# Kernel tuning notes

Hardware: AMD Instinct MI355X
Metric: run time of the kernel (lower is better)

Reference implementation:

```python
import jax, jax.numpy as jnp
import numpy as np

# ---- static config (mirrors init_kwargs) ----
B, N, C_IN, C_OUT = 4, 8192, 128, 256
RATIO = 0.25
M = int(N * RATIO)          # sampled centers per cloud (fps ratio)
RADIUS = 0.1
MAX_NN = 64                 # max_num_neighbors
K = 16                      # num kernel points
D_MID = C_IN // 2           # pre_mlp: in_features -> in_features // 2
KP_EXTENT = RADIUS          # kernel-point influence extent (linear influence)


def setup_inputs() -> dict:
    key = jax.random.key(0)
    ks = jax.random.split(key, 10)
    x = jax.random.normal(ks[0], (B, N, C_IN), jnp.float32)
    pos = jax.random.uniform(ks[1], (B, N, 3), jnp.float32)  # unit cube
    W_pre = jax.random.normal(ks[2], (C_IN, D_MID), jnp.float32) / np.sqrt(C_IN).astype(np.float32)
    b_pre = jnp.zeros((D_MID,), jnp.float32)
    kp_pos = jax.random.normal(ks[3], (K, 3), jnp.float32) * (0.3 * RADIUS)
    kp_W = jax.random.normal(ks[4], (K, D_MID, D_MID), jnp.float32) / np.sqrt(D_MID * K).astype(np.float32)
    W_post = jax.random.normal(ks[5], (D_MID, C_OUT), jnp.float32) / np.sqrt(D_MID).astype(np.float32)
    b_post = jnp.zeros((C_OUT,), jnp.float32)
    W_sc = jax.random.normal(ks[6], (C_IN, C_OUT), jnp.float32) / np.sqrt(C_IN).astype(np.float32)
    b_sc = jnp.zeros((C_OUT,), jnp.float32)
    return dict(x=x, pos=pos, W_pre=W_pre, b_pre=b_pre, kp_pos=kp_pos, kp_W=kp_W,
                W_post=W_post, b_post=b_post, W_sc=W_sc, b_sc=b_sc)


def _fps(p):
    """Farthest point sampling on one cloud p:[N,3] -> idx:[M] (start at point 0)."""
    mind = jnp.sum((p - p[0]) ** 2, axis=-1)  # [N]
    def step(mind, _):
        i = jnp.argmax(mind).astype(jnp.int32)
        mind = jnp.minimum(mind, jnp.sum((p - p[i]) ** 2, axis=-1))
        return mind, i
    _, rest = jax.lax.scan(step, mind, None, length=M - 1)
    return jnp.concatenate([jnp.zeros((1,), jnp.int32), rest])


def reference(x, pos, W_pre, b_pre, kp_pos, kp_W, W_post, b_post, W_sc, b_sc):
    def _cloud(xb, pb):
        # xb:[N,C_IN], pb:[N,3]
        idx = _fps(pb)                                   # [M]
        centers = pb[idx]                                # [M,3]
        # radius neighbor search: nearest MAX_NN, mask to ball of RADIUS
        d2 = jnp.sum((centers[:, None, :] - pb[None, :, :]) ** 2, axis=-1)   # [M,N]
        neg_d2, nn_idx = jax.lax.top_k(-d2, MAX_NN)      # [M,MAX_NN]
        valid = (-neg_d2) <= RADIUS ** 2                 # [M,MAX_NN]
        # pre mlp then gather neighbor features (x_j)
        x_pre = xb @ W_pre + b_pre                       # [N,D_MID]
        x_j = x_pre[nn_idx]                              # [M,MAX_NN,D_MID]
        # kernel-point conv: linear influence of each kernel point
        rel = pb[nn_idx] - centers[:, None, :]           # [M,MAX_NN,3]
        dist = jnp.sqrt(jnp.sum((rel[:, :, None, :] - kp_pos[None, None, :, :]) ** 2, axis=-1) + 1e-12)  # [M,MAX_NN,K]
        infl = jnp.maximum(1.0 - dist / KP_EXTENT, 0.0) * valid[:, :, None]
        # aggregate (sum over neighbors) per kernel point, then contract with kernel weights
        s = jnp.einsum('mek,med->mkd', infl, x_j)        # [M,K,D_MID]
        feat = jnp.einsum('mkd,kdo->mo', s, kp_W)        # [M,D_MID]
        feat = feat @ W_post + b_post                    # [M,C_OUT]
        short = xb[idx] @ W_sc + b_sc                    # residual shortcut on sampled points
        return feat + short, centers

    out_feat, out_pos = jax.vmap(_cloud)(x, pos)         # [B,M,C_OUT], [B,M,3]
    return out_feat, out_pos
```

## Files before the change

### kernel.cpp

```cpp
#include <hip/hip_runtime.h>

#define B_    4
#define N_    8192
#define CIN   128
#define COUT  256
#define M_    2048
#define K_    16
#define DM    64
#define MAXNN 64
#define CAP   128
#define R2    0.01f
#define EXT   0.1f

#define NPRE  1024
#define CONV0 (4 + NPRE)
#define PUB   32

typedef float v2f __attribute__((ext_vector_type(2)));
typedef unsigned long long ull;

__device__ __forceinline__ float d2_exact(float ax, float ay, float az,
                                          float bx, float by, float bz) {
    float dx = ax - bx, dy = ay - by, dz = az - bz;
    return __fadd_rn(__fadd_rn(__fmul_rn(dx, dx), __fmul_rn(dy, dy)), __fmul_rn(dz, dz));
}

#define DPP_STEP2(CTRL)                                                                   \
    {                                                                                     \
        unsigned tlo = (unsigned)__builtin_amdgcn_update_dpp(0, (int)klo, CTRL, 0xF, 0xF, true); \
        unsigned thi = (unsigned)__builtin_amdgcn_update_dpp(0, (int)khi, CTRL, 0xF, 0xF, true); \
        unsigned long long tk = ((unsigned long long)thi << 32) | tlo;                    \
        unsigned long long ck = ((unsigned long long)khi << 32) | klo;                    \
        if (tk > ck) { klo = tlo; khi = thi; }                                            \
    }

__global__ void init_kernel(int* __restrict__ flags) {
    if (threadIdx.x < 8) flags[threadIdx.x] = 0;
}

__global__ __launch_bounds__(512, 2) void mega_kernel(const float* __restrict__ pos,
                                                      int* __restrict__ idx_out,
                                                      float* __restrict__ out_pos,
                                                      const float* __restrict__ x,
                                                      const float* __restrict__ Wp,
                                                      const float* __restrict__ bvec,
                                                      float* __restrict__ xpre,
                                                      const float* __restrict__ kp_pos,
                                                      const float* __restrict__ kp_W,
                                                      const float* __restrict__ W_post,
                                                      const float* __restrict__ b_post,
                                                      const float* __restrict__ W_sc,
                                                      const float* __restrict__ b_sc,
                                                      float* __restrict__ out_feat,
                                                      int* __restrict__ flags) {
    __shared__ union {
        struct { float sx[N_]; float sy[N_]; float sz[N_]; ull slots[2][8]; } f;
        struct { float Ws[CIN * DM]; float xs[32][CIN]; } p;
        struct { int nIdx[CAP]; float nD2[CAP]; int cntS;
                 float infl[MAXNN][K_]; float xj[MAXNN][DM];
                 float sS[K_ * DM]; float featP[4][DM]; float xg[CIN]; } c;
    } sh;

    const int t = threadIdx.x;
    const int blk = blockIdx.x;

    if (blk >= CONV0) {
        const int cid = blk - CONV0;
        const int cb = cid & 3;
        const int cm = cid >> 2;

        if (t == 0) {
            while (__hip_atomic_load(&flags[cb], __ATOMIC_RELAXED, __HIP_MEMORY_SCOPE_AGENT) <= cm ||
                   __hip_atomic_load(&flags[4], __ATOMIC_RELAXED, __HIP_MEMORY_SCOPE_AGENT) < NPRE) {
                __builtin_amdgcn_s_sleep(64);
            }
            __threadfence();
            sh.c.cntS = 0;
        }
        __syncthreads();

        const float* pb = pos + (size_t)cb * N_ * 3;
        const int ctr = idx_out[cb * M_ + cm];
        const float ccx = pb[ctr * 3 + 0], ccy = pb[ctr * 3 + 1], ccz = pb[ctr * 3 + 2];

        for (int j = 0; j < N_ / 512; j++) {
            int n = j * 512 + t;
            float x0 = pb[n * 3 + 0], y0 = pb[n * 3 + 1], z0 = pb[n * 3 + 2];
            float d = d2_exact(x0, y0, z0, ccx, ccy, ccz);
            if (d <= R2) {
                int pp = atomicAdd(&sh.c.cntS, 1);
                if (pp < CAP) { sh.c.nIdx[pp] = n; sh.c.nD2[pp] = d; }
            }
        }
        __syncthreads();
        int cnt = sh.c.cntS; if (cnt > CAP) cnt = CAP;
        if (cnt > MAXNN) {
            if (t == 0) {
                for (int s = 0; s < MAXNN; s++) {
                    int best = s;
                    for (int q = s + 1; q < cnt; q++) {
                        if (sh.c.nD2[q] < sh.c.nD2[best] ||
                            (sh.c.nD2[q] == sh.c.nD2[best] && sh.c.nIdx[q] < sh.c.nIdx[best])) best = q;
                    }
                    float td = sh.c.nD2[best]; sh.c.nD2[best] = sh.c.nD2[s]; sh.c.nD2[s] = td;
                    int ti = sh.c.nIdx[best]; sh.c.nIdx[best] = sh.c.nIdx[s]; sh.c.nIdx[s] = ti;
                }
            }
            __syncthreads();
            cnt = MAXNN;
        }

        if (t < cnt) {
            int n = sh.c.nIdx[t];
            float rx = pb[n * 3 + 0] - ccx, ry = pb[n * 3 + 1] - ccy, rz = pb[n * 3 + 2] - ccz;
#pragma unroll
            for (int k = 0; k < K_; k++) {
                float dx = rx - kp_pos[k * 3 + 0];
                float dy = ry - kp_pos[k * 3 + 1];
                float dz = rz - kp_pos[k * 3 + 2];
                float dist = sqrtf(dx * dx + dy * dy + dz * dz + 1e-12f);
                sh.c.infl[t][k] = fmaxf(1.0f - dist / EXT, 0.0f);
            }
        }
        for (int i = t; i < cnt * DM; i += 512) {
            int e = i >> 6, d = i & 63;
            sh.c.xj[e][d] = xpre[((size_t)cb * N_ + sh.c.nIdx[e]) * DM + d];
        }
        __syncthreads();

        if (t < 256) {
#pragma unroll
            for (int p4 = 0; p4 < 4; p4++) {
                int pair = t + p4 * 256;
                int k = pair >> 6, d = pair & 63;
                float acc = 0.f;
                for (int e = 0; e < cnt; e++) acc = fmaf(sh.c.infl[e][k], sh.c.xj[e][d], acc);
                sh.c.sS[pair] = acc;
            }
        }
        __syncthreads();

        if (t < 256) {
            int dprime = t & 63, ks = t >> 6;
            float acc = 0.f;
            for (int k = ks * 4; k < ks * 4 + 4; k++) {
                const float* kw = kp_W + ((size_t)k * DM) * DM + dprime;
#pragma unroll
                for (int d = 0; d < DM; d++) acc = fmaf(sh.c.sS[k * DM + d], kw[d * DM], acc);
            }
            sh.c.featP[ks][dprime] = acc;
        }
        __syncthreads();
        if (t < DM) sh.c.featP[0][t] = sh.c.featP[0][t] + sh.c.featP[1][t] + sh.c.featP[2][t] + sh.c.featP[3][t];
        if (t < CIN) sh.c.xg[t] = x[((size_t)cb * N_ + ctr) * CIN + t];
        __syncthreads();

        if (t < 256) {
            const int o = t;
            float acc = b_post[o] + b_sc[o];
#pragma unroll 8
            for (int d = 0; d < DM; d++) acc = fmaf(sh.c.featP[0][d], W_post[d * COUT + o], acc);
#pragma unroll 8
            for (int cc = 0; cc < CIN; cc++) acc = fmaf(sh.c.xg[cc], W_sc[cc * COUT + o], acc);
            out_feat[((size_t)(cb * M_ + cm)) * COUT + o] = acc;
        }
        return;
    }

    if (blk >= 4) {
        const size_t rowBase = (size_t)(blk - 4) * 32;
        for (int i = t; i < CIN * DM; i += 512) sh.p.Ws[i] = Wp[i];
        for (int i = t; i < 32 * CIN; i += 512) {
            int r = i >> 7, c = i & 127;
            sh.p.xs[r][c] = x[(rowBase + r) * CIN + c];
        }
        __syncthreads();
        const int col = t & 63, r0 = t >> 6;
        float acc[4];
        float bias = bvec[col];
#pragma unroll
        for (int rr = 0; rr < 4; rr++) acc[rr] = bias;
        for (int c = 0; c < CIN; c++) {
            float w = sh.p.Ws[c * DM + col];
#pragma unroll
            for (int rr = 0; rr < 4; rr++) acc[rr] = fmaf(sh.p.xs[r0 + 8 * rr][c], w, acc[rr]);
        }
#pragma unroll
        for (int rr = 0; rr < 4; rr++) xpre[(rowBase + r0 + 8 * rr) * DM + col] = acc[rr];
        __threadfence();
        __syncthreads();
        if (t == 0) atomicAdd(&flags[4], 1);
        return;
    }

    const int b = blk;
    const float* pb = pos + (size_t)b * N_ * 3;

    v2f px[8], py[8], pz[8], mind[8];
#pragma unroll
    for (int jj = 0; jj < 8; jj++) {
        int n0 = t + (2 * jj) * 512, n1 = n0 + 512;
        float x0 = pb[n0 * 3 + 0], y0 = pb[n0 * 3 + 1], z0 = pb[n0 * 3 + 2];
        float x1 = pb[n1 * 3 + 0], y1 = pb[n1 * 3 + 1], z1 = pb[n1 * 3 + 2];
        px[jj] = (v2f){x0, x1};
        py[jj] = (v2f){y0, y1};
        pz[jj] = (v2f){z0, z1};
        mind[jj] = (v2f){1e30f, 1e30f};
        sh.f.sx[n0] = x0; sh.f.sy[n0] = y0; sh.f.sz[n0] = z0;
        sh.f.sx[n1] = x1; sh.f.sy[n1] = y1; sh.f.sz[n1] = z1;
    }
    float cx = pb[0], cy = pb[1], cz = pb[2];
    if (t == 0) {
        idx_out[b * M_ + 0] = 0;
        float* op = out_pos + ((size_t)(b * M_ + 0)) * 3;
        op[0] = cx; op[1] = cy; op[2] = cz;
    }
    __syncthreads();

    for (int m = 1; m < M_; m++) {
        float bv = -1.0f; int bj = 0;
        {
#pragma clang fp contract(off)
            v2f cx2 = (v2f){cx, cx}, cy2 = (v2f){cy, cy}, cz2 = (v2f){cz, cz};
#pragma unroll
            for (int jj = 0; jj < 8; jj++) {
                v2f dx = px[jj] - cx2, dy = py[jj] - cy2, dz = pz[jj] - cz2;
                v2f d = (dx * dx + dy * dy) + dz * dz;
                v2f mo = mind[jj];
                float n0 = fminf(mo.x, d.x);
                float n1 = fminf(mo.y, d.y);
                mind[jj] = (v2f){n0, n1};
                if (n0 > bv) { bv = n0; bj = 2 * jj; }
                if (n1 > bv) { bv = n1; bj = 2 * jj + 1; }
            }
        }
        const int bn = t + (bj << 9);
        unsigned klo = ~(unsigned)bn;
        unsigned khi = __float_as_uint(bv);

        DPP_STEP2(0x111)
        DPP_STEP2(0x112)
        DPP_STEP2(0x114)
        DPP_STEP2(0x118)
        DPP_STEP2(0x142)
        DPP_STEP2(0x143)

        ull* sl = sh.f.slots[m & 1];
        if ((t & 63) == 63) sl[t >> 6] = ((ull)khi << 32) | klo;
        __syncthreads();

        ull k0 = sl[0], k1 = sl[1], k2 = sl[2], k3 = sl[3];
        ull k4 = sl[4], k5 = sl[5], k6 = sl[6], k7 = sl[7];
        ull a0 = k0 > k1 ? k0 : k1;
        ull a1 = k2 > k3 ? k2 : k3;
        ull a2 = k4 > k5 ? k4 : k5;
        ull a3 = k6 > k7 ? k6 : k7;
        ull b0 = a0 > a1 ? a0 : a1;
        ull b1 = a2 > a3 ? a2 : a3;
        ull kk = b0 > b1 ? b0 : b1;

        const unsigned widx = ~(unsigned)(kk & 0xFFFFFFFFull);
        cx = sh.f.sx[widx]; cy = sh.f.sy[widx]; cz = sh.f.sz[widx];
        if (t == 0) {
            idx_out[b * M_ + m] = (int)widx;
            float* op = out_pos + ((size_t)(b * M_ + m)) * 3;
            op[0] = cx; op[1] = cy; op[2] = cz;
            if ((m & (PUB - 1)) == (PUB - 1)) {
                __threadfence();
                __hip_atomic_store(&flags[b], m + 1, __ATOMIC_RELAXED, __HIP_MEMORY_SCOPE_AGENT);
            }
        }
    }
}

extern "C" void kernel_launch(void* const* d_in, const int* in_sizes, int n_in,
                              void* d_out, int out_size, void* d_ws, size_t ws_size,
                              hipStream_t stream) {
    const float* x      = (const float*)d_in[0];
    const float* pos    = (const float*)d_in[1];
    const float* W_pre  = (const float*)d_in[2];
    const float* b_pre  = (const float*)d_in[3];
    const float* kp_pos = (const float*)d_in[4];
    const float* kp_W   = (const float*)d_in[5];
    const float* W_post = (const float*)d_in[6];
    const float* b_post = (const float*)d_in[7];
    const float* W_sc   = (const float*)d_in[8];
    const float* b_sc   = (const float*)d_in[9];

    float* out_feat = (float*)d_out;
    float* out_pos  = (float*)d_out + (size_t)B_ * M_ * COUT;

    int*   idxs  = (int*)d_ws;
    int*   flags = (int*)((char*)d_ws + 48 * 1024);
    float* xpre  = (float*)((char*)d_ws + 64 * 1024);

    init_kernel<<<1, 64, 0, stream>>>(flags);
    mega_kernel<<<CONV0 + B_ * M_, 512, 0, stream>>>(pos, idxs, out_pos,
                                                     x, W_pre, b_pre, xpre,
                                                     kp_pos, kp_W, W_post, b_post,
                                                     W_sc, b_sc, out_feat, flags);
}
```

Baseline: 1.917 ms.

## Pack two FPS clouds per 1024-thread block with per-group spin barriers

Blocks grow to 1024 threads and each FPS block now handles two clouds, one per 512-thread half. Each half replaces __syncthreads with an LDS atomic counter and spin-wait, so the two clouds' argmax reductions do not block each other. The per-cloud LDS copy of positions is removed and winning center coordinates are read from global memory. This reduces the FPS stage to two blocks and tries to overlap the two serial chains within one CU. The risks are global-load latency on the serial critical path, spin-wait contention, and idle threads in the conv and pre-MLP blocks. The launch bound of 1024 threads with 4 blocks per multiprocessor may also constrain registers.

```diff
diff --git a/kernel.cpp b/kernel.cpp
--- a/kernel.cpp
+++ b/kernel.cpp
@@ -13,7 +13,7 @@
 #define EXT   0.1f
 
 #define NPRE  1024
-#define CONV0 (4 + NPRE)
+#define CONV0 (2 + NPRE)
 #define PUB   32
 
 typedef float v2f __attribute__((ext_vector_type(2)));
@@ -38,23 +38,23 @@
     if (threadIdx.x < 8) flags[threadIdx.x] = 0;
 }
 
-__global__ __launch_bounds__(512, 2) void mega_kernel(const float* __restrict__ pos,
-                                                      int* __restrict__ idx_out,
-                                                      float* __restrict__ out_pos,
-                                                      const float* __restrict__ x,
-                                                      const float* __restrict__ Wp,
-                                                      const float* __restrict__ bvec,
-                                                      float* __restrict__ xpre,
-                                                      const float* __restrict__ kp_pos,
-                                                      const float* __restrict__ kp_W,
-                                                      const float* __restrict__ W_post,
-                                                      const float* __restrict__ b_post,
-                                                      const float* __restrict__ W_sc,
-                                                      const float* __restrict__ b_sc,
-                                                      float* __restrict__ out_feat,
-                                                      int* __restrict__ flags) {
+__global__ __launch_bounds__(1024, 4) void mega_kernel(const float* __restrict__ pos,
+                                                       int* __restrict__ idx_out,
+                                                       float* __restrict__ out_pos,
+                                                       const float* __restrict__ x,
+                                                       const float* __restrict__ Wp,
+                                                       const float* __restrict__ bvec,
+                                                       float* __restrict__ xpre,
+                                                       const float* __restrict__ kp_pos,
+                                                       const float* __restrict__ kp_W,
+                                                       const float* __restrict__ W_post,
+                                                       const float* __restrict__ b_post,
+                                                       const float* __restrict__ W_sc,
+                                                       const float* __restrict__ b_sc,
+                                                       float* __restrict__ out_feat,
+                                                       int* __restrict__ flags) {
     __shared__ union {
-        struct { float sx[N_]; float sy[N_]; float sz[N_]; ull slots[2][8]; } f;
+        struct { ull slots[2][2][8]; unsigned cnt[2][32]; } f;
         struct { float Ws[CIN * DM]; float xs[32][CIN]; } p;
         struct { int nIdx[CAP]; float nD2[CAP]; int cntS;
                  float infl[MAXNN][K_]; float xj[MAXNN][DM];
@@ -83,13 +83,15 @@
         const int ctr = idx_out[cb * M_ + cm];
         const float ccx = pb[ctr * 3 + 0], ccy = pb[ctr * 3 + 1], ccz = pb[ctr * 3 + 2];
 
-        for (int j = 0; j < N_ / 512; j++) {
-            int n = j * 512 + t;
-            float x0 = pb[n * 3 + 0], y0 = pb[n * 3 + 1], z0 = pb[n * 3 + 2];
-            float d = d2_exact(x0, y0, z0, ccx, ccy, ccz);
-            if (d <= R2) {
-                int pp = atomicAdd(&sh.c.cntS, 1);
-                if (pp < CAP) { sh.c.nIdx[pp] = n; sh.c.nD2[pp] = d; }
+        if (t < 512) {
+            for (int j = 0; j < N_ / 512; j++) {
+                int n = j * 512 + t;
+                float x0 = pb[n * 3 + 0], y0 = pb[n * 3 + 1], z0 = pb[n * 3 + 2];
+                float d = d2_exact(x0, y0, z0, ccx, ccy, ccz);
+                if (d <= R2) {
+                    int pp = atomicAdd(&sh.c.cntS, 1);
+                    if (pp < CAP) { sh.c.nIdx[pp] = n; sh.c.nD2[pp] = d; }
+                }
             }
         }
         __syncthreads();
@@ -122,9 +124,11 @@
                 sh.c.infl[t][k] = fmaxf(1.0f - dist / EXT, 0.0f);
             }
         }
-        for (int i = t; i < cnt * DM; i += 512) {
-            int e = i >> 6, d = i & 63;
-            sh.c.xj[e][d] = xpre[((size_t)cb * N_ + sh.c.nIdx[e]) * DM + d];
+        if (t < 512) {
+            for (int i = t; i < cnt * DM; i += 512) {
+                int e = i >> 6, d = i & 63;
+                sh.c.xj[e][d] = xpre[((size_t)cb * N_ + sh.c.nIdx[e]) * DM + d];
+            }
         }
         __syncthreads();
 
@@ -167,55 +171,62 @@
         return;
     }
 
-    if (blk >= 4) {
-        const size_t rowBase = (size_t)(blk - 4) * 32;
-        for (int i = t; i < CIN * DM; i += 512) sh.p.Ws[i] = Wp[i];
-        for (int i = t; i < 32 * CIN; i += 512) {
-            int r = i >> 7, c = i & 127;
-            sh.p.xs[r][c] = x[(rowBase + r) * CIN + c];
-        }
-        __syncthreads();
-        const int col = t & 63, r0 = t >> 6;
-        float acc[4];
-        float bias = bvec[col];
-#pragma unroll
-        for (int rr = 0; rr < 4; rr++) acc[rr] = bias;
-        for (int c = 0; c < CIN; c++) {
-            float w = sh.p.Ws[c * DM + col];
-#pragma unroll
-            for (int rr = 0; rr < 4; rr++) acc[rr] = fmaf(sh.p.xs[r0 + 8 * rr][c], w, acc[rr]);
-        }
-#pragma unroll
-        for (int rr = 0; rr < 4; rr++) xpre[(rowBase + r0 + 8 * rr) * DM + col] = acc[rr];
+    if (blk >= 2) {
+        const size_t rowBase = (size_t)(blk - 2) * 32;
+        if (t < 512) {
+            for (int i = t; i < CIN * DM; i += 512) sh.p.Ws[i] = Wp[i];
+            for (int i = t; i < 32 * CIN; i += 512) {
+                int r = i >> 7, c = i & 127;
+                sh.p.xs[r][c] = x[(rowBase + r) * CIN + c];
+            }
+        }
+        __syncthreads();
+        if (t < 512) {
+            const int col = t & 63, r0 = (t >> 6) & 7;
+            float acc[4];
+            float bias = bvec[col];
+#pragma unroll
+            for (int rr = 0; rr < 4; rr++) acc[rr] = bias;
+            for (int c = 0; c < CIN; c++) {
+                float w = sh.p.Ws[c * DM + col];
+#pragma unroll
+                for (int rr = 0; rr < 4; rr++) acc[rr] = fmaf(sh.p.xs[r0 + 8 * rr][c], w, acc[rr]);
+            }
+#pragma unroll
+            for (int rr = 0; rr < 4; rr++) xpre[(rowBase + r0 + 8 * rr) * DM + col] = acc[rr];
+        }
         __threadfence();
         __syncthreads();
         if (t == 0) atomicAdd(&flags[4], 1);
         return;
     }
 
-    const int b = blk;
+    const int cg = t >> 9;
+    const int lt = t & 511;
+    const int b = 2 * blk + cg;
     const float* pb = pos + (size_t)b * N_ * 3;
 
     v2f px[8], py[8], pz[8], mind[8];
 #pragma unroll
     for (int jj = 0; jj < 8; jj++) {
-        int n0 = t + (2 * jj) * 512, n1 = n0 + 512;
-        float x0 = pb[n0 * 3 + 0], y0 = pb[n0 * 3 + 1], z0 = pb[n0 * 3 + 2];
-        float x1 = pb[n1 * 3 + 0], y1 = pb[n1 * 3 + 1], z1 = pb[n1 * 3 + 2];
-        px[jj] = (v2f){x0, x1};
-        py[jj] = (v2f){y0, y1};
-        pz[jj] = (v2f){z0, z1};
+        int n0 = lt + (2 * jj) * 512, n1 = n0 + 512;
+        px[jj] = (v2f){pb[n0 * 3 + 0], pb[n1 * 3 + 0]};
+        py[jj] = (v2f){pb[n0 * 3 + 1], pb[n1 * 3 + 1]};
+        pz[jj] = (v2f){pb[n0 * 3 + 2], pb[n1 * 3 + 2]};
         mind[jj] = (v2f){1e30f, 1e30f};
-        sh.f.sx[n0] = x0; sh.f.sy[n0] = y0; sh.f.sz[n0] = z0;
-        sh.f.sx[n1] = x1; sh.f.sy[n1] = y1; sh.f.sz[n1] = z1;
     }
     float cx = pb[0], cy = pb[1], cz = pb[2];
-    if (t == 0) {
+    if (lt == 0) {
+        sh.f.cnt[cg][0] = 0;
         idx_out[b * M_ + 0] = 0;
         float* op = out_pos + ((size_t)(b * M_ + 0)) * 3;
         op[0] = cx; op[1] = cy; op[2] = cz;
     }
     __syncthreads();
+
+    if (cg == 1) __builtin_amdgcn_s_sleep(16);
+
+    unsigned* cnt = &sh.f.cnt[cg][0];
 
     for (int m = 1; m < M_; m++) {
         float bv = -1.0f; int bj = 0;
@@ -234,7 +245,7 @@
                 if (n1 > bv) { bv = n1; bj = 2 * jj + 1; }
             }
         }
-        const int bn = t + (bj << 9);
+        const int bn = lt + (bj << 9);
         unsigned klo = ~(unsigned)bn;
         unsigned khi = __float_as_uint(bv);
 
@@ -245,9 +256,13 @@
         DPP_STEP2(0x142)
         DPP_STEP2(0x143)
 
-        ull* sl = sh.f.slots[m & 1];
-        if ((t & 63) == 63) sl[t >> 6] = ((ull)khi << 32) | klo;
-        __syncthreads();
+        ull* sl = sh.f.slots[cg][m & 1];
+        if ((lt & 63) == 63) {
+            sl[lt >> 6] = ((ull)khi << 32) | klo;
+            __hip_atomic_fetch_add(cnt, 1u, __ATOMIC_RELEASE, __HIP_MEMORY_SCOPE_WORKGROUP);
+        }
+        while (__hip_atomic_load(cnt, __ATOMIC_ACQUIRE, __HIP_MEMORY_SCOPE_WORKGROUP)
+               < (unsigned)(8 * m)) { }
 
         ull k0 = sl[0], k1 = sl[1], k2 = sl[2], k3 = sl[3];
         ull k4 = sl[4], k5 = sl[5], k6 = sl[6], k7 = sl[7];
@@ -260,8 +275,9 @@
         ull kk = b0 > b1 ? b0 : b1;
 
         const unsigned widx = ~(unsigned)(kk & 0xFFFFFFFFull);
-        cx = sh.f.sx[widx]; cy = sh.f.sy[widx]; cz = sh.f.sz[widx];
-        if (t == 0) {
+        const float* cp = pb + (size_t)widx * 3;
+        cx = cp[0]; cy = cp[1]; cz = cp[2];
+        if (lt == 0) {
             idx_out[b * M_ + m] = (int)widx;
             float* op = out_pos + ((size_t)(b * M_ + m)) * 3;
             op[0] = cx; op[1] = cy; op[2] = cz;
@@ -295,8 +311,8 @@
     float* xpre  = (float*)((char*)d_ws + 64 * 1024);
 
     init_kernel<<<1, 64, 0, stream>>>(flags);
-    mega_kernel<<<CONV0 + B_ * M_, 512, 0, stream>>>(pos, idxs, out_pos,
-                                                     x, W_pre, b_pre, xpre,
-                                                     kp_pos, kp_W, W_post, b_post,
-                                                     W_sc, b_sc, out_feat, flags);
+    mega_kernel<<<CONV0 + B_ * M_, 1024, 0, stream>>>(pos, idxs, out_pos,
+                                                      x, W_pre, b_pre, xpre,
+                                                      kp_pos, kp_W, W_post, b_post,
+                                                      W_sc, b_sc, out_feat, flags);
 }
```

After: 3.697 ms. +92.9%, slower.
